# Optimization experiments

Measured on AMD Instinct MI355X. Metric: run time of the kernel, lower is better.

The kernel has to match this reference:

```python
import jax, jax.numpy as jnp
import numpy as np

ALPHA = 0.9        # LIF membrane decay
THRESH = 1.0       # spike threshold
SURR_BETA = 4.0    # surrogate-gradient sharpness
TIME_STEPS = 32    # fabric simulation steps per token position


def _spike(v):
    """Heaviside spike with sigmoid surrogate gradient (straight-through)."""
    hard = (v >= THRESH).astype(v.dtype)
    soft = jax.nn.sigmoid(SURR_BETA * (v - THRESH))
    return soft + jax.lax.stop_gradient(hard - soft)


def setup_inputs() -> dict:
    key = jax.random.key(0)
    k0, k1, k2, k3 = jax.random.split(key, 4)
    B, S, D = 8, 128, 512
    N_in, N_out = 1024, 1024
    embeddings = jax.random.normal(k0, (B, S, D), jnp.float32)
    W_in = jax.random.normal(k1, (D, N_in), jnp.float32) / np.sqrt(D).astype(np.float32)
    b_in = jnp.zeros((N_in,), jnp.float32)
    W_conn = jax.random.normal(k2, (N_in, N_out), jnp.float32) / np.sqrt(N_in).astype(np.float32)
    W_out = jax.random.normal(k3, (N_out, D), jnp.float32) / np.sqrt(N_out).astype(np.float32)
    b_out = jnp.zeros((D,), jnp.float32)
    return {"embeddings": embeddings, "W_in": W_in, "b_in": b_in,
            "W_conn": W_conn, "W_out": W_out, "b_out": b_out}


def reference(embeddings, W_in, b_in, W_conn, W_out, b_out):
    B, S, D = embeddings.shape
    N_in = W_in.shape[1]
    N_out = W_conn.shape[1]

    # embed_to_snn + relu, precomputed for all positions: [B, S, N_in]
    snn_input = jax.nn.relu(jnp.einsum('bsd,dn->bsn', embeddings, W_in) + b_in)

    def time_step(carry, _):
        v_in, v_out, pos_input = carry
        # input population: leaky integrate external current
        v_in = ALPHA * v_in + pos_input
        s_in = _spike(v_in)
        v_in = v_in - s_in * THRESH          # soft reset
        # output population: driven by input-population spikes
        v_out = ALPHA * v_out + s_in @ W_conn
        s_out = _spike(v_out)
        v_out = v_out - s_out * THRESH
        n_spk = jax.lax.stop_gradient(s_in.sum() + s_out.sum())
        return (v_in, v_out, pos_input), (s_out, n_spk)

    def pos_step(carry, pos_input):
        v_in, v_out = carry
        (v_in, v_out, _), (s_outs, n_spks) = jax.lax.scan(
            time_step, (v_in, v_out, pos_input), None, length=TIME_STEPS)
        spike_acc = s_outs.sum(axis=0)       # [B, N_out], sum over timesteps
        pos_out = spike_acc @ W_out + b_out  # snn_to_embed
        return (v_in, v_out), (pos_out, n_spks.sum())

    v0_in = jnp.zeros((B, N_in), embeddings.dtype)
    v0_out = jnp.zeros((B, N_out), embeddings.dtype)
    snn_seq = jnp.swapaxes(snn_input, 0, 1)  # [S, B, N_in]: scan over positions
    _, (outs, spk_counts) = jax.lax.scan(pos_step, (v0_in, v0_out), snn_seq)

    output_embeddings = jnp.swapaxes(outs, 0, 1)  # [B, S, D]
    total_neurons = N_in + N_out
    spike_rate = spk_counts.sum() / (B * S * total_neurons * TIME_STEPS)
    return output_embeddings, spike_rate
```

## Files before the change

### kernel.cpp

```cpp
#include <hip/hip_runtime.h>
#include <stdint.h>

#define B 8
#define S 128
#define D 512
#define NIN 1024
#define NOUT 1024
#define T 32

typedef __attribute__((ext_vector_type(8))) short short8;
typedef __attribute__((ext_vector_type(4))) float floatx4;

__global__ __launch_bounds__(256) void k_gemm(const float* __restrict__ A,
                                              const float* __restrict__ Bm,
                                              const float* __restrict__ bias,
                                              float* __restrict__ C,
                                              int M, int N, int K, int relu)
{
    __shared__ float As[16][64];
    __shared__ float Bs[16][64];
    const int tid = threadIdx.x;
    const int bx = blockIdx.x, by = blockIdx.y;
    const int tx = tid & 15, ty = tid >> 4;
    const int ar = tid >> 2, ak = (tid & 3) << 2;
    const int bk = tid >> 4, bc = (tid & 15) << 2;
    float acc[4][4] = {{0.f,0.f,0.f,0.f},{0.f,0.f,0.f,0.f},
                       {0.f,0.f,0.f,0.f},{0.f,0.f,0.f,0.f}};
    for (int k0 = 0; k0 < K; k0 += 16) {
        float4 a4 = *(const float4*)(A + (size_t)(by*64 + ar)*K + k0 + ak);
        float4 b4 = *(const float4*)(Bm + (size_t)(k0 + bk)*N + bx*64 + bc);
        __syncthreads();
        As[ak+0][ar] = a4.x; As[ak+1][ar] = a4.y;
        As[ak+2][ar] = a4.z; As[ak+3][ar] = a4.w;
        *(float4*)&Bs[bk][bc] = b4;
        __syncthreads();
        #pragma unroll
        for (int kk = 0; kk < 16; ++kk) {
            float4 av = *(const float4*)&As[kk][ty << 2];
            float4 bv = *(const float4*)&Bs[kk][tx << 2];
            acc[0][0] = fmaf(av.x, bv.x, acc[0][0]);
            acc[0][1] = fmaf(av.x, bv.y, acc[0][1]);
            acc[0][2] = fmaf(av.x, bv.z, acc[0][2]);
            acc[0][3] = fmaf(av.x, bv.w, acc[0][3]);
            acc[1][0] = fmaf(av.y, bv.x, acc[1][0]);
            acc[1][1] = fmaf(av.y, bv.y, acc[1][1]);
            acc[1][2] = fmaf(av.y, bv.z, acc[1][2]);
            acc[1][3] = fmaf(av.y, bv.w, acc[1][3]);
            acc[2][0] = fmaf(av.z, bv.x, acc[2][0]);
            acc[2][1] = fmaf(av.z, bv.y, acc[2][1]);
            acc[2][2] = fmaf(av.z, bv.z, acc[2][2]);
            acc[2][3] = fmaf(av.z, bv.w, acc[2][3]);
            acc[3][0] = fmaf(av.w, bv.x, acc[3][0]);
            acc[3][1] = fmaf(av.w, bv.y, acc[3][1]);
            acc[3][2] = fmaf(av.w, bv.z, acc[3][2]);
            acc[3][3] = fmaf(av.w, bv.w, acc[3][3]);
        }
    }
    const int row0 = by*64 + (ty << 2), col0 = bx*64 + (tx << 2);
    float4 bb = *(const float4*)(bias + col0);
    #pragma unroll
    for (int i = 0; i < 4; ++i) {
        float4 o;
        o.x = acc[i][0] + bb.x; o.y = acc[i][1] + bb.y;
        o.z = acc[i][2] + bb.z; o.w = acc[i][3] + bb.w;
        if (relu) {
            o.x = fmaxf(o.x, 0.f); o.y = fmaxf(o.y, 0.f);
            o.z = fmaxf(o.z, 0.f); o.w = fmaxf(o.w, 0.f);
        }
        *(float4*)(C + (size_t)(row0 + i)*N + col0) = o;
    }
}

__global__ __launch_bounds__(256) void k_lif_inA(const float* __restrict__ snn,
                                                 unsigned int* __restrict__ sbits,
                                                 unsigned int* __restrict__ counters)
{
    const int tid = blockIdx.x * 256 + threadIdx.x;
    const int b = tid >> 10, n = tid & (NIN - 1);
    const float* cur = snn + (size_t)(b * S) * NIN + n;
    float v = 0.f;
    int cnt = 0;
    float I = cur[0];
    for (int s = 0; s < S; ++s) {
        const float In = (s + 1 < S) ? cur[(size_t)(s + 1) * NIN] : 0.f;
        unsigned int bits = 0u;
        #pragma unroll
        for (int t = 0; t < T; ++t) {
            v = __fadd_rn(__fmul_rn(0.9f, v), I);
            const bool sp = (v >= 1.0f);
            v = sp ? (v - 1.0f) : v;
            bits |= (sp ? 1u : 0u) << t;
        }
        sbits[(size_t)(b * S + s) * NIN + n] = bits;
        cnt += __popc(bits);
        I = In;
    }
    atomicAdd(counters, (unsigned int)cnt);
}

__global__ __launch_bounds__(256) void k_lif_inB(const unsigned int* __restrict__ sbits,
                                                 unsigned long long* __restrict__ masks)
{
    const int bs = blockIdx.x;
    const int w = threadIdx.x >> 6, lane = threadIdx.x & 63;
    #pragma unroll
    for (int i = 0; i < 4; ++i) {
        const int wq = w * 4 + i;
        const unsigned int bits = sbits[(size_t)bs * NIN + wq * 64 + lane];
        #pragma unroll
        for (int t = 0; t < T; ++t) {
            const unsigned long long m = __ballot((bits >> t) & 1u);
            if (lane == 0)
                masks[((size_t)bs * T + t) * 16 + wq] = m;
        }
    }
}

__global__ __launch_bounds__(256) void k_prep(const float* __restrict__ Wc,
                                              unsigned short* __restrict__ WhT,
                                              unsigned short* __restrict__ WlT)
{
    __shared__ float tile[64][65];
    const int k0 = blockIdx.x * 64, n0 = blockIdx.y * 64;
    const int tx = threadIdx.x & 63, ty = threadIdx.x >> 6;
    #pragma unroll
    for (int p = 0; p < 16; ++p) {
        const int kl = p*4 + ty;
        tile[kl][tx] = Wc[(size_t)(k0 + kl) * NOUT + n0 + tx];
    }
    __syncthreads();
    #pragma unroll
    for (int p = 0; p < 16; ++p) {
        const int nl = p*4 + ty;
        const float w = tile[tx][nl];
        const unsigned int u  = __float_as_uint(w);
        const unsigned int hb = (u + 0x7FFFu + ((u >> 16) & 1u)) & 0xFFFF0000u;
        const float hif = __uint_as_float(hb);
        const float lo  = w - hif;
        const unsigned int ul = __float_as_uint(lo);
        const unsigned short lob = (unsigned short)((ul + 0x7FFFu + ((ul >> 16) & 1u)) >> 16);
        WhT[(size_t)(n0 + nl) * NIN + k0 + tx] = (unsigned short)(hb >> 16);
        WlT[(size_t)(n0 + nl) * NIN + k0 + tx] = lob;
    }
}

__global__ __launch_bounds__(256, 2) void k_conn_mfma(
    const uint4* __restrict__ masks128,
    const unsigned short* __restrict__ WhT,
    const unsigned short* __restrict__ WlT,
    float* __restrict__ Iout, int s0, int P)
{
    __shared__ unsigned short Bsm[2 * 4 * 8 * 512];

    const int tid = threadIdx.x;
    const int w = tid >> 6, lane = tid & 63;
    const int r16 = lane & 15, q = lane >> 4;
    const int PT = P * T;
    const int rowblk = blockIdx.x * 256 + w * 64;
    const int cb = blockIdx.y * 128;

    const uint4* aptr[4];
    #pragma unroll
    for (int f = 0; f < 4; ++f) {
        const int r = rowblk + f*16 + r16;
        const int b = r / PT;
        const int within = r - b * PT;
        const int grow = (b * S + s0) * T + within;
        aptr[f] = masks128 + (size_t)grow * 8;
    }

    const int lane_s = tid & 63, s0slot = tid >> 6;
    unsigned int boff[16];
    #pragma unroll
    for (int i = 0; i < 16; ++i) {
        const int slot = s0slot + 4 * i;
        const int cfrag = slot & 7, kc = (slot >> 3) & 3;
        boff[i] = (unsigned int)((cfrag * 16 + (lane_s & 15)) * NIN
                                 + kc * 32 + (lane_s >> 4) * 8);
    }
    const unsigned short* whb = WhT + (size_t)cb * NIN;
    const unsigned short* wlb = WlT + (size_t)cb * NIN;
    unsigned short* bdst = Bsm + 8 * tid;

    floatx4 acc[4][8];
    #pragma unroll
    for (int f = 0; f < 4; ++f)
        #pragma unroll
        for (int c = 0; c < 8; ++c)
            acc[f][c] = (floatx4){0.f, 0.f, 0.f, 0.f};

    const unsigned short* bp = Bsm + (size_t)lane * 8;

    for (int ch = 0; ch < 8; ++ch) {
        __syncthreads();
        #pragma unroll
        for (int i = 0; i < 8; ++i)
            *(uint4*)(bdst + i * 2048) = *(const uint4*)(whb + boff[i] + ch * 128);
        #pragma unroll
        for (int i = 8; i < 16; ++i)
            *(uint4*)(bdst + i * 2048) = *(const uint4*)(wlb + boff[i] + ch * 128);
        uint4 aw[4];
        #pragma unroll
        for (int f = 0; f < 4; ++f) aw[f] = aptr[f][ch];
        __syncthreads();

        #pragma unroll
        for (int kc = 0; kc < 4; ++kc) {
            short8 af[4];
            #pragma unroll
            for (int f = 0; f < 4; ++f) {
                const unsigned int word = (kc == 0) ? aw[f].x : (kc == 1) ? aw[f].y
                                         : (kc == 2) ? aw[f].z : aw[f].w;
                const unsigned int byte = (word >> (q * 8)) & 0xFFu;
                union { unsigned int u[4]; short8 s; } A;
                #pragma unroll
                for (int j = 0; j < 4; ++j)
                    A.u[j] = (((byte >> (2*j)) & 1u) ? 0x3F80u : 0u)
                           | (((byte >> (2*j+1)) & 1u) ? 0x3F800000u : 0u);
                af[f] = A.s;
            }
            #pragma unroll
            for (int c = 0; c < 8; ++c) {
                const short8 bh = *(const short8*)(bp + ((kc * 8 + c) << 9));
                const short8 bl = *(const short8*)(bp + ((32 * 512) + ((kc * 8 + c) << 9)));
                #pragma unroll
                for (int f = 0; f < 4; ++f) {
                    acc[f][c] = __builtin_amdgcn_mfma_f32_16x16x32_bf16(af[f], bh, acc[f][c], 0, 0, 0);
                    acc[f][c] = __builtin_amdgcn_mfma_f32_16x16x32_bf16(af[f], bl, acc[f][c], 0, 0, 0);
                }
            }
        }
    }

    #pragma unroll
    for (int f = 0; f < 4; ++f) {
        const int row = rowblk + f*16 + q*4;
        #pragma unroll
        for (int c = 0; c < 8; ++c) {
            const int col = cb + c*16 + r16;
            #pragma unroll
            for (int i = 0; i < 4; ++i)
                Iout[(size_t)(row + i) * NOUT + col] = acc[f][c][i];
        }
    }
}

__global__ __launch_bounds__(256) void k_lif_out(const float* __restrict__ Iout,
                                                 float* __restrict__ vstate,
                                                 float* __restrict__ sacc_out,
                                                 unsigned int* __restrict__ counters,
                                                 int s0, int P, int init)
{
    const int tid = blockIdx.x * 256 + threadIdx.x;
    const int b = tid >> 10, n = tid & (NOUT - 1);
    const int Tc = P * T;
    float v = init ? 0.f : vstate[tid];
    const float* ip = Iout + (size_t)b * Tc * NOUT + n;
    int cnt = 0;

    float cur[T];
    #pragma unroll
    for (int t = 0; t < T; ++t) cur[t] = ip[(size_t)t * NOUT];

    for (int sl = 0; sl < P; ++sl) {
        float nxt[T];
        const bool has = (sl + 1 < P);
        if (has) {
            const float* ip2 = ip + (size_t)(sl + 1) * T * NOUT;
            #pragma unroll
            for (int t = 0; t < T; ++t) nxt[t] = ip2[(size_t)t * NOUT];
        }
        float sacc = 0.f;
        #pragma unroll
        for (int t = 0; t < T; ++t) {
            v = __fadd_rn(__fmul_rn(0.9f, v), cur[t]);
            const bool sp = (v >= 1.0f);
            v = sp ? (v - 1.0f) : v;
            sacc += sp ? 1.f : 0.f;
            cnt += sp ? 1 : 0;
        }
        sacc_out[(size_t)(b*S + s0 + sl) * NOUT + n] = sacc;
        if (has) {
            #pragma unroll
            for (int t = 0; t < T; ++t) cur[t] = nxt[t];
        }
    }
    vstate[tid] = v;
    atomicAdd(counters + 1, (unsigned int)cnt);
}

__global__ void k_init(unsigned int* c)
{
    if (threadIdx.x < 2) c[threadIdx.x] = 0u;
}

__global__ void k_rate(const unsigned int* __restrict__ c, float* __restrict__ out)
{
    if (threadIdx.x == 0 && blockIdx.x == 0) {
        const float total = (float)c[0] + (float)c[1];
        out[0] = total / (float)(B * S * (NIN + NOUT) * T);
    }
}

extern "C" void kernel_launch(void* const* d_in, const int* in_sizes, int n_in,
                              void* d_out, int out_size, void* d_ws, size_t ws_size,
                              hipStream_t stream)
{
    const float* E    = (const float*)d_in[0];
    const float* Win  = (const float*)d_in[1];
    const float* bin  = (const float*)d_in[2];
    const float* Wc   = (const float*)d_in[3];
    const float* Wout = (const float*)d_in[4];
    const float* bout = (const float*)d_in[5];
    float* out = (float*)d_out;

    char* w = (char*)d_ws;
    float* snn              = (float*)(w);
    unsigned short* WhT     = (unsigned short*)(w);
    unsigned short* WlT     = (unsigned short*)(w + (2 << 20));
    unsigned long long* msk = (unsigned long long*)(w + (4 << 20));
    float* sacc             = (float*)(w + (8 << 20));
    unsigned int* sbits     = (unsigned int*)(w + (8 << 20));
    float* vst              = (float*)(w + (12 << 20));
    unsigned int* cnt       = (unsigned int*)(w + (12 << 20) + (64 << 10));
    float* Iout             = (float*)(w + (13 << 20));

    const size_t base = (size_t)13 << 20;
    const size_t avail = (ws_size > base) ? (ws_size - base) : 0;
    int P = 1;
    if      (avail >= (size_t)B * 128 * T * NOUT * 4) P = 128;
    else if (avail >= (size_t)B *  16 * T * NOUT * 4) P = 16;
    else if (avail >= (size_t)B *   4 * T * NOUT * 4) P = 4;

    k_init<<<1, 64, 0, stream>>>(cnt);

    dim3 g1(NIN / 64, (B * S) / 64);
    k_gemm<<<g1, 256, 0, stream>>>(E, Win, bin, snn, B * S, NIN, D, 1);

    k_lif_inA<<<32, 256, 0, stream>>>(snn, sbits, cnt);
    k_lif_inB<<<B * S, 256, 0, stream>>>(sbits, msk);

    dim3 gp(NIN / 64, NOUT / 64);
    k_prep<<<gp, 256, 0, stream>>>(Wc, WhT, WlT);

    for (int c = 0; c < S / P; ++c) {
        dim3 gc((B * P * T) / 256, NOUT / 128);
        k_conn_mfma<<<gc, 256, 0, stream>>>((const uint4*)msk, WhT, WlT, Iout, c * P, P);
        k_lif_out<<<32, 256, 0, stream>>>(Iout, vst, sacc, cnt, c * P, P, c == 0 ? 1 : 0);
    }

    dim3 g2(D / 64, (B * S) / 64);
    k_gemm<<<g2, 256, 0, stream>>>(sacc, Wout, bout, out, B * S, D, NOUT, 0);

    k_rate<<<1, 64, 0, stream>>>(cnt, out + (size_t)B * S * D);
}
```

Baseline: 493.8 us.

## Retile conn MFMA to 128x64 per wave with direct LDS loads, deepen LIF prefetch

The connectivity MFMA kernel now gives each wave 128 rows by 64 columns (2x2 wave grid) instead of 64 rows by 128 columns, so each B fragment read from LDS feeds more MFMAs. B tiles are staged with global_load_lds when the builtin is available, bypassing registers. Spike-mask unpacking uses a multiply trick instead of selects. The output LIF kernel prefetches two positions ahead rather than one. The cost is more accumulator and A-fragment registers per wave, which may hurt occupancy under launch_bounds(256,2), and more registers in the LIF kernel.

Measured after the change: 611.9 us. 1.24x slower.

```diff
diff --git a/kernel.cpp b/kernel.cpp
--- a/kernel.cpp
+++ b/kernel.cpp
@@ -155,76 +155,88 @@
     const int tid = threadIdx.x;
     const int w = tid >> 6, lane = tid & 63;
     const int r16 = lane & 15, q = lane >> 4;
+    const int wr = w >> 1, wc = w & 1;
     const int PT = P * T;
-    const int rowblk = blockIdx.x * 256 + w * 64;
+    const int rowwave = blockIdx.x * 256 + wr * 128;
     const int cb = blockIdx.y * 128;
-
-    const uint4* aptr[4];
-    #pragma unroll
-    for (int f = 0; f < 4; ++f) {
-        const int r = rowblk + f*16 + r16;
+    const int cw = cb + wc * 64;
+
+    const uint4* aptr[8];
+    #pragma unroll
+    for (int f = 0; f < 8; ++f) {
+        const int r = rowwave + f*16 + r16;
         const int b = r / PT;
-        const int within = r - b * PT;
-        const int grow = (b * S + s0) * T + within;
+        const int grow = (b * S + s0) * T + (r - b * PT);
         aptr[f] = masks128 + (size_t)grow * 8;
     }
 
-    const int lane_s = tid & 63, s0slot = tid >> 6;
-    unsigned int boff[16];
-    #pragma unroll
-    for (int i = 0; i < 16; ++i) {
-        const int slot = s0slot + 4 * i;
-        const int cfrag = slot & 7, kc = (slot >> 3) & 3;
-        boff[i] = (unsigned int)((cfrag * 16 + (lane_s & 15)) * NIN
-                                 + kc * 32 + (lane_s >> 4) * 8);
-    }
-    const unsigned short* whb = WhT + (size_t)cb * NIN;
-    const unsigned short* wlb = WlT + (size_t)cb * NIN;
-    unsigned short* bdst = Bsm + 8 * tid;
-
-    floatx4 acc[4][8];
-    #pragma unroll
-    for (int f = 0; f < 4; ++f)
-        #pragma unroll
-        for (int c = 0; c < 8; ++c)
+    const unsigned short* bsrc[8];
+    #pragma unroll
+    for (int i = 0; i < 8; ++i) {
+        const int slot = w + 4 * i;
+        const int kc = (slot >> 3) & 3, cf = slot & 7;
+        bsrc[i] = WhT + (size_t)(cb + cf*16 + r16) * NIN + kc * 32 + q * 8;
+    }
+    const size_t loDelta = (size_t)(WlT - WhT);
+
+    floatx4 acc[8][4];
+    #pragma unroll
+    for (int f = 0; f < 8; ++f)
+        #pragma unroll
+        for (int c = 0; c < 4; ++c)
             acc[f][c] = (floatx4){0.f, 0.f, 0.f, 0.f};
 
     const unsigned short* bp = Bsm + (size_t)lane * 8;
 
     for (int ch = 0; ch < 8; ++ch) {
         __syncthreads();
-        #pragma unroll
-        for (int i = 0; i < 8; ++i)
-            *(uint4*)(bdst + i * 2048) = *(const uint4*)(whb + boff[i] + ch * 128);
-        #pragma unroll
-        for (int i = 8; i < 16; ++i)
-            *(uint4*)(bdst + i * 2048) = *(const uint4*)(wlb + boff[i] + ch * 128);
-        uint4 aw[4];
-        #pragma unroll
-        for (int f = 0; f < 4; ++f) aw[f] = aptr[f][ch];
+#if __has_builtin(__builtin_amdgcn_global_load_lds)
+        #pragma unroll
+        for (int i = 0; i < 8; ++i) {
+            __builtin_amdgcn_global_load_lds(
+                (const __attribute__((address_space(1))) void*)(bsrc[i] + ch * 128),
+                (__attribute__((address_space(3))) void*)&Bsm[(w + 4*i) * 512],
+                16, 0, 0);
+            __builtin_amdgcn_global_load_lds(
+                (const __attribute__((address_space(1))) void*)(bsrc[i] + loDelta + ch * 128),
+                (__attribute__((address_space(3))) void*)&Bsm[(32 + w + 4*i) * 512],
+                16, 0, 0);
+        }
+#else
+        #pragma unroll
+        for (int i = 0; i < 8; ++i) {
+            const uint4 h = *(const uint4*)(bsrc[i] + ch * 128);
+            const uint4 l = *(const uint4*)(bsrc[i] + loDelta + ch * 128);
+            *(uint4*)&Bsm[(w + 4*i) * 512 + lane * 8] = h;
+            *(uint4*)&Bsm[(32 + w + 4*i) * 512 + lane * 8] = l;
+        }
+#endif
+        uint4 aw[8];
+        #pragma unroll
+        for (int f = 0; f < 8; ++f) aw[f] = aptr[f][ch];
         __syncthreads();
 
         #pragma unroll
         for (int kc = 0; kc < 4; ++kc) {
-            short8 af[4];
-            #pragma unroll
-            for (int f = 0; f < 4; ++f) {
+            short8 af[8];
+            #pragma unroll
+            for (int f = 0; f < 8; ++f) {
                 const unsigned int word = (kc == 0) ? aw[f].x : (kc == 1) ? aw[f].y
                                          : (kc == 2) ? aw[f].z : aw[f].w;
                 const unsigned int byte = (word >> (q * 8)) & 0xFFu;
+                const unsigned int t2 = byte | (byte << 15);
                 union { unsigned int u[4]; short8 s; } A;
                 #pragma unroll
                 for (int j = 0; j < 4; ++j)
-                    A.u[j] = (((byte >> (2*j)) & 1u) ? 0x3F80u : 0u)
-                           | (((byte >> (2*j+1)) & 1u) ? 0x3F800000u : 0u);
+                    A.u[j] = ((t2 >> (2*j)) & 0x00010001u) * 0x3F80u;
                 af[f] = A.s;
             }
             #pragma unroll
-            for (int c = 0; c < 8; ++c) {
-                const short8 bh = *(const short8*)(bp + ((kc * 8 + c) << 9));
-                const short8 bl = *(const short8*)(bp + ((32 * 512) + ((kc * 8 + c) << 9)));
+            for (int c = 0; c < 4; ++c) {
+                const short8 bh = *(const short8*)(bp + ((kc * 8 + wc * 4 + c) << 9));
+                const short8 bl = *(const short8*)(bp + ((32 + kc * 8 + wc * 4 + c) << 9));
                 #pragma unroll
-                for (int f = 0; f < 4; ++f) {
+                for (int f = 0; f < 8; ++f) {
                     acc[f][c] = __builtin_amdgcn_mfma_f32_16x16x32_bf16(af[f], bh, acc[f][c], 0, 0, 0);
                     acc[f][c] = __builtin_amdgcn_mfma_f32_16x16x32_bf16(af[f], bl, acc[f][c], 0, 0, 0);
                 }
@@ -233,11 +245,11 @@
     }
 
     #pragma unroll
-    for (int f = 0; f < 4; ++f) {
-        const int row = rowblk + f*16 + q*4;
-        #pragma unroll
-        for (int c = 0; c < 8; ++c) {
-            const int col = cb + c*16 + r16;
+    for (int f = 0; f < 8; ++f) {
+        const int row = rowwave + f*16 + q*4;
+        #pragma unroll
+        for (int c = 0; c < 4; ++c) {
+            const int col = cw + c*16 + r16;
             #pragma unroll
             for (int i = 0; i < 4; ++i)
                 Iout[(size_t)(row + i) * NOUT + col] = acc[f][c][i];
@@ -258,32 +270,53 @@
     const float* ip = Iout + (size_t)b * Tc * NOUT + n;
     int cnt = 0;
 
-    float cur[T];
-    #pragma unroll
-    for (int t = 0; t < T; ++t) cur[t] = ip[(size_t)t * NOUT];
-
-    for (int sl = 0; sl < P; ++sl) {
-        float nxt[T];
-        const bool has = (sl + 1 < P);
-        if (has) {
-            const float* ip2 = ip + (size_t)(sl + 1) * T * NOUT;
-            #pragma unroll
-            for (int t = 0; t < T; ++t) nxt[t] = ip2[(size_t)t * NOUT];
-        }
-        float sacc = 0.f;
-        #pragma unroll
-        for (int t = 0; t < T; ++t) {
-            v = __fadd_rn(__fmul_rn(0.9f, v), cur[t]);
-            const bool sp = (v >= 1.0f);
-            v = sp ? (v - 1.0f) : v;
-            sacc += sp ? 1.f : 0.f;
-            cnt += sp ? 1 : 0;
-        }
-        sacc_out[(size_t)(b*S + s0 + sl) * NOUT + n] = sacc;
-        if (has) {
-            #pragma unroll
-            for (int t = 0; t < T; ++t) cur[t] = nxt[t];
-        }
+    float c0[T], c1[T];
+    #pragma unroll
+    for (int t = 0; t < T; ++t) c0[t] = ip[(size_t)t * NOUT];
+    if (P > 1) {
+        const float* p1 = ip + (size_t)T * NOUT;
+        #pragma unroll
+        for (int t = 0; t < T; ++t) c1[t] = p1[(size_t)t * NOUT];
+    }
+
+    for (int sl = 0; sl < P; sl += 2) {
+        float n0[T], n1[T];
+        if (sl + 2 < P) {
+            const float* p = ip + (size_t)(sl + 2) * T * NOUT;
+            #pragma unroll
+            for (int t = 0; t < T; ++t) n0[t] = p[(size_t)t * NOUT];
+        }
+        if (sl + 3 < P) {
+            const float* p = ip + (size_t)(sl + 3) * T * NOUT;
+            #pragma unroll
+            for (int t = 0; t < T; ++t) n1[t] = p[(size_t)t * NOUT];
+        }
+        {
+            float sacc = 0.f;
+            #pragma unroll
+            for (int t = 0; t < T; ++t) {
+                v = __fadd_rn(__fmul_rn(0.9f, v), c0[t]);
+                const bool sp = (v >= 1.0f);
+                v = sp ? (v - 1.0f) : v;
+                sacc += sp ? 1.f : 0.f;
+                cnt += sp ? 1 : 0;
+            }
+            sacc_out[(size_t)(b*S + s0 + sl) * NOUT + n] = sacc;
+        }
+        if (sl + 1 < P) {
+            float sacc = 0.f;
+            #pragma unroll
+            for (int t = 0; t < T; ++t) {
+                v = __fadd_rn(__fmul_rn(0.9f, v), c1[t]);
+                const bool sp = (v >= 1.0f);
+                v = sp ? (v - 1.0f) : v;
+                sacc += sp ? 1.f : 0.f;
+                cnt += sp ? 1 : 0;
+            }
+            sacc_out[(size_t)(b*S + s0 + sl + 1) * NOUT + n] = sacc;
+        }
+        #pragma unroll
+        for (int t = 0; t < T; ++t) { c0[t] = n0[t]; c1[t] = n1[t]; }
     }
     vstate[tid] = v;
     atomicAdd(counters + 1, (unsigned int)cnt);
```

## Retile spike-mask MFMA GEMM to 2x2 waves with direct global-to-LDS loads

Applied to the files above, without the earlier changes.

Changes the connection GEMM's wave tiling from 4 row-waves by 128 columns to a 2x2 grid where each wave covers 128 rows by 64 columns. The K chunk is halved to 64, so LDS use drops. Weight tiles now go straight from global memory to LDS via global_load_lds, and the spike masks are staged through shared memory instead of per-lane registers. Mask-to-bf16 expansion uses a multiply trick instead of selects. The squarer wave tile raises reuse of A and B fragments, at the cost of twice as many sync iterations and heavier register pressure from 8x4 accumulators.

After: 484.7 us. No clear change (-1.8%).

```diff
diff --git a/kernel.cpp b/kernel.cpp
--- a/kernel.cpp
+++ b/kernel.cpp
@@ -145,86 +145,84 @@
 }
 
 __global__ __launch_bounds__(256, 2) void k_conn_mfma(
-    const uint4* __restrict__ masks128,
+    const unsigned long long* __restrict__ masks64,
     const unsigned short* __restrict__ WhT,
     const unsigned short* __restrict__ WlT,
     float* __restrict__ Iout, int s0, int P)
 {
-    __shared__ unsigned short Bsm[2 * 4 * 8 * 512];
+    __shared__ unsigned short Bsm[32 * 512];
+    __shared__ unsigned long long Msm[256];
 
     const int tid = threadIdx.x;
     const int w = tid >> 6, lane = tid & 63;
     const int r16 = lane & 15, q = lane >> 4;
+    const int wr = w >> 1, wc = w & 1;
     const int PT = P * T;
-    const int rowblk = blockIdx.x * 256 + w * 64;
+    const int rowwave = blockIdx.x * 256 + wr * 128;
     const int cb = blockIdx.y * 128;
-
-    const uint4* aptr[4];
-    #pragma unroll
-    for (int f = 0; f < 4; ++f) {
-        const int r = rowblk + f*16 + r16;
+    const int cw = cb + wc * 64;
+
+    const unsigned long long* mrow;
+    {
+        const int r = blockIdx.x * 256 + tid;
         const int b = r / PT;
-        const int within = r - b * PT;
-        const int grow = (b * S + s0) * T + within;
-        aptr[f] = masks128 + (size_t)grow * 8;
-    }
-
-    const int lane_s = tid & 63, s0slot = tid >> 6;
-    unsigned int boff[16];
-    #pragma unroll
-    for (int i = 0; i < 16; ++i) {
-        const int slot = s0slot + 4 * i;
-        const int cfrag = slot & 7, kc = (slot >> 3) & 3;
-        boff[i] = (unsigned int)((cfrag * 16 + (lane_s & 15)) * NIN
-                                 + kc * 32 + (lane_s >> 4) * 8);
-    }
-    const unsigned short* whb = WhT + (size_t)cb * NIN;
-    const unsigned short* wlb = WlT + (size_t)cb * NIN;
-    unsigned short* bdst = Bsm + 8 * tid;
-
-    floatx4 acc[4][8];
-    #pragma unroll
-    for (int f = 0; f < 4; ++f)
-        #pragma unroll
-        for (int c = 0; c < 8; ++c)
+        const int grow = (b * S + s0) * T + (r - b * PT);
+        mrow = masks64 + (size_t)grow * 16;
+    }
+
+    const unsigned short* bsrc[8];
+    #pragma unroll
+    for (int i = 0; i < 8; ++i) {
+        const int slot = w + 4 * i;
+        const int mat = slot >> 4, rest = slot & 15;
+        const int kc2 = rest >> 3, cf = rest & 7;
+        bsrc[i] = (mat ? WlT : WhT)
+                + (size_t)(cb + cf * 16 + r16) * NIN + kc2 * 32 + q * 8;
+    }
+
+    floatx4 acc[8][4];
+    #pragma unroll
+    for (int f = 0; f < 8; ++f)
+        #pragma unroll
+        for (int c = 0; c < 4; ++c)
             acc[f][c] = (floatx4){0.f, 0.f, 0.f, 0.f};
 
     const unsigned short* bp = Bsm + (size_t)lane * 8;
-
-    for (int ch = 0; ch < 8; ++ch) {
+    const unsigned int* Msm32 = (const unsigned int*)Msm;
+
+    for (int ch = 0; ch < 16; ++ch) {
         __syncthreads();
         #pragma unroll
-        for (int i = 0; i < 8; ++i)
-            *(uint4*)(bdst + i * 2048) = *(const uint4*)(whb + boff[i] + ch * 128);
-        #pragma unroll
-        for (int i = 8; i < 16; ++i)
-            *(uint4*)(bdst + i * 2048) = *(const uint4*)(wlb + boff[i] + ch * 128);
-        uint4 aw[4];
-        #pragma unroll
-        for (int f = 0; f < 4; ++f) aw[f] = aptr[f][ch];
+        for (int i = 0; i < 8; ++i) {
+            __builtin_amdgcn_global_load_lds(
+                (const __attribute__((address_space(1))) void*)(bsrc[i] + ch * 64),
+                (__attribute__((address_space(3))) void*)&Bsm[(w + 4 * i) * 512],
+                16, 0, 0);
+        }
+        Msm[tid] = mrow[ch];
         __syncthreads();
 
         #pragma unroll
-        for (int kc = 0; kc < 4; ++kc) {
-            short8 af[4];
-            #pragma unroll
-            for (int f = 0; f < 4; ++f) {
-                const unsigned int word = (kc == 0) ? aw[f].x : (kc == 1) ? aw[f].y
-                                         : (kc == 2) ? aw[f].z : aw[f].w;
+        for (int kc2 = 0; kc2 < 2; ++kc2) {
+            short8 af[8];
+            #pragma unroll
+            for (int f = 0; f < 8; ++f) {
+                const int row = wr * 128 + f * 16 + r16;
+                const unsigned int word = Msm32[row * 2 + kc2];
                 const unsigned int byte = (word >> (q * 8)) & 0xFFu;
+                const unsigned int t2 = byte | (byte << 15);
                 union { unsigned int u[4]; short8 s; } A;
                 #pragma unroll
                 for (int j = 0; j < 4; ++j)
-                    A.u[j] = (((byte >> (2*j)) & 1u) ? 0x3F80u : 0u)
-                           | (((byte >> (2*j+1)) & 1u) ? 0x3F800000u : 0u);
+                    A.u[j] = ((t2 >> (2 * j)) & 0x00010001u) * 0x3F80u;
                 af[f] = A.s;
             }
             #pragma unroll
-            for (int c = 0; c < 8; ++c) {
-                const short8 bh = *(const short8*)(bp + ((kc * 8 + c) << 9));
-                const short8 bl = *(const short8*)(bp + ((32 * 512) + ((kc * 8 + c) << 9)));
+            for (int c = 0; c < 4; ++c) {
+                const short8 bh = *(const short8*)(bp + ((kc2 * 8 + wc * 4 + c) << 9));
+                const short8 bl = *(const short8*)(bp + ((16 + kc2 * 8 + wc * 4 + c) << 9));
                 #pragma unroll
-                for (int f = 0; f < 4; ++f) {
+                for (int f = 0; f < 8; ++f) {
                     acc[f][c] = __builtin_amdgcn_mfma_f32_16x16x32_bf16(af[f], bh, acc[f][c], 0, 0, 0);
                     acc[f][c] = __builtin_amdgcn_mfma_f32_16x16x32_bf16(af[f], bl, acc[f][c], 0, 0, 0);
                 }
@@ -233,11 +231,11 @@
     }
 
     #pragma unroll
-    for (int f = 0; f < 4; ++f) {
-        const int row = rowblk + f*16 + q*4;
-        #pragma unroll
-        for (int c = 0; c < 8; ++c) {
-            const int col = cb + c*16 + r16;
+    for (int f = 0; f < 8; ++f) {
+        const int row = rowwave + f * 16 + q * 4;
+        #pragma unroll
+        for (int c = 0; c < 4; ++c) {
+            const int col = cw + c * 16 + r16;
             #pragma unroll
             for (int i = 0; i < 4; ++i)
                 Iout[(size_t)(row + i) * NOUT + col] = acc[f][c][i];
@@ -345,7 +343,7 @@
 
     for (int c = 0; c < S / P; ++c) {
         dim3 gc((B * P * T) / 256, NOUT / 128);
-        k_conn_mfma<<<gc, 256, 0, stream>>>((const uint4*)msk, WhT, WlT, Iout, c * P, P);
+        k_conn_mfma<<<gc, 256, 0, stream>>>(msk, WhT, WlT, Iout, c * P, P);
         k_lif_out<<<32, 256, 0, stream>>>(Iout, vst, sacc, cnt, c * P, P, c == 0 ? 1 : 0);
     }
 
```
